# Kernel optimization log

Measured on AMD Instinct MI355X. Metric: run time of the kernel, lower is better.

The kernel has to match this reference:

```python
import jax, jax.numpy as jnp
import numpy as np


def setup_inputs() -> dict:
    key = jax.random.key(0)
    inputs = jax.random.normal(key, (4096, 8192), dtype=jnp.float32)
    return {"inputs": inputs, "k": 512}


def reference(inputs, k):
    # Original: kth_smallest = sort_ascending(inputs)[..., n-1-k]
    # i.e. the (k+1)-th largest value per row. Equivalent via top_k.
    # Keep only elements STRICTLY greater than that threshold.
    thresh = jax.lax.top_k(inputs, k + 1)[0][..., -1]  # [batch]
    mask = (inputs > thresh[:, None]).astype(inputs.dtype)
    return inputs * mask
```

## Files before the change

kernel.cpp:

```cpp
#include <hip/hip_runtime.h>
#include <stdint.h>


constexpr int COLS  = 8192;
constexpr int TPB   = 256;
constexpr int EPT   = COLS / TPB;
constexpr int VPT   = EPT / 4;
constexpr int NBIN0 = 2048;
constexpr int CAP   = 2048;

__device__ __forceinline__ uint32_t map_f32(uint32_t u) {
  return (u & 0x80000000u) ? ~u : (u | 0x80000000u);
}
__device__ __forceinline__ float unmap_f32(uint32_t m) {
  return __uint_as_float((m & 0x80000000u) ? (m ^ 0x80000000u) : ~m);
}
__device__ __forceinline__ uint32_t bin11(uint32_t u) {
  const uint32_t s = u >> 21;
  return (u & 0x80000000u) ? (0x7FFu ^ s) : (s | 0x400u);
}
__device__ __forceinline__ uint32_t hswz(uint32_t w) {
  return w ^ ((w >> 3) & 0x1Cu);
}

__device__ __forceinline__ void bar_lds() {
  asm volatile("s_waitcnt lgkmcnt(0)" ::: "memory");
  __builtin_amdgcn_s_barrier();
  asm volatile("" ::: "memory");
}

template <int RPB>
__global__ __launch_bounds__(TPB, 4)
void ksparse_kernel(const float* __restrict__ in, const int* __restrict__ kptr,
                    float* __restrict__ out) {
  __shared__ __align__(16) uint32_t hist[2 * NBIN0];
  __shared__ uint32_t th[3 * 128];
  __shared__ uint32_t s_packed;
  __shared__ uint32_t s_cnt;
  __shared__ uint32_t s_T;

  const int t    = threadIdx.x;
  const int wave = t >> 6;
  const int lane = t & 63;
  const size_t row0 = (size_t)blockIdx.x * RPB;

  const uint32_t kbase = (uint32_t)(*kptr) + 1u;

  float4 v[2][VPT];

  {
    const float4* inp = (const float4*)(in + row0 * COLS);
#pragma unroll
    for (int i = 0; i < VPT; ++i) v[0][i] = inp[t + i * TPB];
  }

#pragma unroll
  for (int r = 0; r < RPB; ++r) {
    const int cb = r & 1;

    if (r + 1 < RPB) {
      const float4* inp = (const float4*)(in + (row0 + (size_t)(r + 1)) * COLS);
#pragma unroll
      for (int i = 0; i < VPT; ++i) v[cb ^ 1][i] = inp[t + i * TPB];
    }

    uint4* h4 = (uint4*)hist;
#pragma unroll
    for (int i = 0; i < (2 * NBIN0 / 4) / TPB; ++i)
      h4[t + i * TPB] = make_uint4(0u, 0u, 0u, 0u);
    th[t] = 0u;
    if (t < 128) th[256 + t] = 0u;
    if (t == 0) { s_packed = 0u; s_cnt = 0u; }
    bar_lds();

    uint32_t* h = &hist[(wave >> 1) * NBIN0];
#pragma unroll
    for (int i = 0; i < VPT; ++i) {
      atomicAdd(&h[hswz(bin11(__float_as_uint(v[cb][i].x)))], 1u);
      atomicAdd(&h[hswz(bin11(__float_as_uint(v[cb][i].y)))], 1u);
      atomicAdd(&h[hswz(bin11(__float_as_uint(v[cb][i].z)))], 1u);
      atomicAdd(&h[hswz(bin11(__float_as_uint(v[cb][i].w)))], 1u);
    }
    bar_lds();

    if (wave == 0) {
      const uint4* r0 = (const uint4*)&hist[0];
      const uint4* r1 = (const uint4*)&hist[NBIN0];
      uint32_t qs[8];
      uint32_t total = 0;
#pragma unroll
      for (int q = 0; q < 8; ++q) {
        const uint32_t Qs = (uint32_t)(8 * lane + q) ^ (uint32_t)(lane & 7);
        const uint4 a = r0[Qs];
        const uint4 b = r1[Qs];
        qs[q] = (a.x + b.x) + (a.y + b.y) + (a.z + b.z) + (a.w + b.w);
        total += qs[q];
      }
      uint32_t s = total;
#pragma unroll
      for (int off = 1; off < 64; off <<= 1) {
        const uint32_t tmp = __shfl_down(s, off, 64);
        s += (lane + off < 64) ? tmp : 0u;
      }
      const unsigned long long mb = __ballot(s >= kbase);
      const int lstar = 63 - __builtin_clzll(mb);
      if (lane == lstar) {
        uint32_t run = s - total;
        int qq = -1; uint32_t qab = 0;
#pragma unroll
        for (int q = 7; q >= 0; --q) {
          const uint32_t nrun = run + qs[q];
          if (qq < 0 && nrun >= kbase) { qq = q; qab = run; }
          run = nrun;
        }
        const uint32_t Qs = (uint32_t)(8 * lane + qq) ^ (uint32_t)(lane & 7);
        const uint4 a = r0[Qs];
        const uint4 b = r1[Qs];
        const uint32_t c1 = a.y + b.y, c2 = a.z + b.z, c3 = a.w + b.w;
        const uint32_t s3 = qab + c3;
        const uint32_t s2 = s3 + c2, s1 = s2 + c1;
        uint32_t e, above;
        if (s3 >= kbase)      { e = 3u; above = qab; }
        else if (s2 >= kbase) { e = 2u; above = s3; }
        else if (s1 >= kbase) { e = 1u; above = s2; }
        else                  { e = 0u; above = s1; }
        const uint32_t d0 = (uint32_t)(lane * 32 + qq * 4) + e;
        s_packed = (d0 << 14) | above;
      }
    }
    bar_lds();

    const uint32_t pk = s_packed;
    const uint32_t d0 = pk >> 14;

    uint32_t* cand = &hist[NBIN0];
#pragma unroll
    for (int i = 0; i < VPT; ++i) {
      uint32_t u;
      u = __float_as_uint(v[cb][i].x);
      if (bin11(u) == d0) { const uint32_t x = atomicAdd(&s_cnt, 1u); if (x < CAP) cand[x] = map_f32(u) & 0x1FFFFFu; }
      u = __float_as_uint(v[cb][i].y);
      if (bin11(u) == d0) { const uint32_t x = atomicAdd(&s_cnt, 1u); if (x < CAP) cand[x] = map_f32(u) & 0x1FFFFFu; }
      u = __float_as_uint(v[cb][i].z);
      if (bin11(u) == d0) { const uint32_t x = atomicAdd(&s_cnt, 1u); if (x < CAP) cand[x] = map_f32(u) & 0x1FFFFFu; }
      u = __float_as_uint(v[cb][i].w);
      if (bin11(u) == d0) { const uint32_t x = atomicAdd(&s_cnt, 1u); if (x < CAP) cand[x] = map_f32(u) & 0x1FFFFFu; }
    }
    bar_lds();

    if (wave == 0) {
      const uint32_t Cc = (s_cnt < (uint32_t)CAP) ? s_cnt : (uint32_t)CAP;
      uint32_t kk = kbase - (pk & 0x3FFFu);
      uint32_t tpref = 0;
#pragma unroll 1
      for (int j = 0; j < 3; ++j) {
        const int dsh = 14 - 7 * j;
        uint32_t* thj = &th[j * 128];
        for (uint32_t idx = (uint32_t)lane; idx < Cc; idx += 64u) {
          const uint32_t c = cand[idx];
          const bool ok = (j == 0) || ((c >> (dsh + 7)) == tpref);
          if (ok) atomicAdd(&thj[(c >> dsh) & 127u], 1u);
        }
        const uint32_t a = thj[lane], b = thj[64 + lane];
        uint32_t sb = b, sa = a;
#pragma unroll
        for (int off = 1; off < 64; off <<= 1) {
          const uint32_t t1 = __shfl_down(sb, off, 64);
          const uint32_t t2 = __shfl_down(sa, off, 64);
          const bool inr = (lane + off < 64);
          sb += inr ? t1 : 0u;
          sa += inr ? t2 : 0u;
        }
        const uint32_t tb = __shfl(sb, 0, 64);
        sa += tb;
        const unsigned long long mbj = __ballot(sb >= kk);
        uint32_t d, ab;
        if (mbj) {
          const int hb = 63 - __builtin_clzll(mbj);
          const uint32_t nx = __shfl(sb, (hb + 1) & 63, 64);
          d = 64u + (uint32_t)hb;
          ab = (hb == 63) ? 0u : nx;
        } else {
          const unsigned long long ma = __ballot(sa >= kk);
          const int ha = 63 - __builtin_clzll(ma);
          const uint32_t nx = __shfl(sa, (ha + 1) & 63, 64);
          d = (uint32_t)ha;
          ab = (ha == 63) ? tb : nx;
        }
        tpref = (tpref << 7) | d;
        kk -= ab;
      }
      if (lane == 0) s_T = (d0 << 21) | tpref;
    }
    bar_lds();

    const float thr = unmap_f32(s_T);
    float4* op = (float4*)(out + (row0 + (size_t)r) * COLS);
#pragma unroll
    for (int i = 0; i < VPT; ++i) {
      float4 w;
      w.x = (v[cb][i].x > thr) ? v[cb][i].x : 0.0f;
      w.y = (v[cb][i].y > thr) ? v[cb][i].y : 0.0f;
      w.z = (v[cb][i].z > thr) ? v[cb][i].z : 0.0f;
      w.w = (v[cb][i].w > thr) ? v[cb][i].w : 0.0f;
      op[t + i * TPB] = w;
    }
  }
}

extern "C" void kernel_launch(void* const* d_in, const int* in_sizes, int n_in,
                              void* d_out, int out_size, void* d_ws, size_t ws_size,
                              hipStream_t stream) {
  const float* in  = (const float*)d_in[0];
  const int*   k   = (const int*)d_in[1];
  float*       out = (float*)d_out;
  int rows = in_sizes[0] / COLS;
  if (rows < 1) rows = 1;
  if ((rows & 3) == 0) {
    ksparse_kernel<4><<<rows / 4, TPB, 0, stream>>>(in, k, out);
  } else {
    ksparse_kernel<1><<<rows, TPB, 0, stream>>>(in, k, out);
  }
}
```

Measured before the change: 283.0 us.

## Prefetch next row via direct global-to-LDS loads instead of register double buffer

Replaces the register double buffer (two float4[8] arrays per thread) with a 32 KB LDS staging buffer filled by global_load_lds. The next row is issued into LDS once the current row has been read into registers for the histogram, which lowers register pressure. The cost is much more LDS per block, so fewer blocks fit on a CU, and the occupancy hint in launch_bounds is dropped. Correctness now depends on manual vmcnt/lgkmcnt waits, and the vmcnt(8) wait is fragile because it assumes a fixed count of outstanding stores versus loads.

Result: faster. 262.4 us (-7.3%).

```diff
diff --git a/kernel.cpp b/kernel.cpp
--- a/kernel.cpp
+++ b/kernel.cpp
@@ -4,8 +4,7 @@
 
 constexpr int COLS  = 8192;
 constexpr int TPB   = 256;
-constexpr int EPT   = COLS / TPB;
-constexpr int VPT   = EPT / 4;
+constexpr int VPT   = 8;
 constexpr int NBIN0 = 2048;
 constexpr int CAP   = 2048;
 
@@ -29,11 +28,27 @@
   asm volatile("" ::: "memory");
 }
 
+__device__ __forceinline__ void gl2lds16(const float* g, float* l) {
+  __builtin_amdgcn_global_load_lds(
+      (const __attribute__((address_space(1))) void*)g,
+      (__attribute__((address_space(3))) void*)l, 16, 0, 0);
+}
+
+__device__ __forceinline__ void stage_row(const float* __restrict__ rowp,
+                                          float* stage, int wave, int lane) {
+  const float* g = rowp + (wave << 11) + (lane << 2);
+  float* l = stage + (wave << 11);
+#pragma unroll
+  for (int i = 0; i < VPT; ++i)
+    gl2lds16(g + i * 256, l + i * 256);
+}
+
 template <int RPB>
-__global__ __launch_bounds__(TPB, 4)
+__global__ __launch_bounds__(TPB)
 void ksparse_kernel(const float* __restrict__ in, const int* __restrict__ kptr,
                     float* __restrict__ out) {
   __shared__ __align__(16) uint32_t hist[2 * NBIN0];
+  __shared__ __align__(16) float    stage[COLS];
   __shared__ uint32_t th[3 * 128];
   __shared__ uint32_t s_packed;
   __shared__ uint32_t s_cnt;
@@ -46,40 +61,35 @@
 
   const uint32_t kbase = (uint32_t)(*kptr) + 1u;
 
-  float4 v[2][VPT];
-
-  {
-    const float4* inp = (const float4*)(in + row0 * COLS);
-#pragma unroll
-    for (int i = 0; i < VPT; ++i) v[0][i] = inp[t + i * TPB];
-  }
+  stage_row(in + row0 * COLS, stage, wave, lane);
 
 #pragma unroll
   for (int r = 0; r < RPB; ++r) {
-    const int cb = r & 1;
-
-    if (r + 1 < RPB) {
-      const float4* inp = (const float4*)(in + (row0 + (size_t)(r + 1)) * COLS);
-#pragma unroll
-      for (int i = 0; i < VPT; ++i) v[cb ^ 1][i] = inp[t + i * TPB];
-    }
-
     uint4* h4 = (uint4*)hist;
 #pragma unroll
-    for (int i = 0; i < (2 * NBIN0 / 4) / TPB; ++i)
+    for (int i = 0; i < 4; ++i)
       h4[t + i * TPB] = make_uint4(0u, 0u, 0u, 0u);
     th[t] = 0u;
     if (t < 128) th[256 + t] = 0u;
     if (t == 0) { s_packed = 0u; s_cnt = 0u; }
     bar_lds();
 
+    if (r == 0) asm volatile("s_waitcnt vmcnt(0)" ::: "memory");
+
+    float4 v[VPT];
     uint32_t* h = &hist[(wave >> 1) * NBIN0];
+    const float4* sq = (const float4*)stage + (wave << 9) + lane;
 #pragma unroll
     for (int i = 0; i < VPT; ++i) {
-      atomicAdd(&h[hswz(bin11(__float_as_uint(v[cb][i].x)))], 1u);
-      atomicAdd(&h[hswz(bin11(__float_as_uint(v[cb][i].y)))], 1u);
-      atomicAdd(&h[hswz(bin11(__float_as_uint(v[cb][i].z)))], 1u);
-      atomicAdd(&h[hswz(bin11(__float_as_uint(v[cb][i].w)))], 1u);
+      v[i] = sq[i << 6];
+      atomicAdd(&h[hswz(bin11(__float_as_uint(v[i].x)))], 1u);
+      atomicAdd(&h[hswz(bin11(__float_as_uint(v[i].y)))], 1u);
+      atomicAdd(&h[hswz(bin11(__float_as_uint(v[i].z)))], 1u);
+      atomicAdd(&h[hswz(bin11(__float_as_uint(v[i].w)))], 1u);
+    }
+    if (r + 1 < RPB) {
+      asm volatile("s_waitcnt lgkmcnt(0)" ::: "memory");
+      stage_row(in + (row0 + (size_t)(r + 1)) * COLS, stage, wave, lane);
     }
     bar_lds();
 
@@ -137,13 +147,13 @@
 #pragma unroll
     for (int i = 0; i < VPT; ++i) {
       uint32_t u;
-      u = __float_as_uint(v[cb][i].x);
-      if (bin11(u) == d0) { const uint32_t x = atomicAdd(&s_cnt, 1u); if (x < CAP) cand[x] = map_f32(u) & 0x1FFFFFu; }
-      u = __float_as_uint(v[cb][i].y);
-      if (bin11(u) == d0) { const uint32_t x = atomicAdd(&s_cnt, 1u); if (x < CAP) cand[x] = map_f32(u) & 0x1FFFFFu; }
-      u = __float_as_uint(v[cb][i].z);
-      if (bin11(u) == d0) { const uint32_t x = atomicAdd(&s_cnt, 1u); if (x < CAP) cand[x] = map_f32(u) & 0x1FFFFFu; }
-      u = __float_as_uint(v[cb][i].w);
+      u = __float_as_uint(v[i].x);
+      if (bin11(u) == d0) { const uint32_t x = atomicAdd(&s_cnt, 1u); if (x < CAP) cand[x] = map_f32(u) & 0x1FFFFFu; }
+      u = __float_as_uint(v[i].y);
+      if (bin11(u) == d0) { const uint32_t x = atomicAdd(&s_cnt, 1u); if (x < CAP) cand[x] = map_f32(u) & 0x1FFFFFu; }
+      u = __float_as_uint(v[i].z);
+      if (bin11(u) == d0) { const uint32_t x = atomicAdd(&s_cnt, 1u); if (x < CAP) cand[x] = map_f32(u) & 0x1FFFFFu; }
+      u = __float_as_uint(v[i].w);
       if (bin11(u) == d0) { const uint32_t x = atomicAdd(&s_cnt, 1u); if (x < CAP) cand[x] = map_f32(u) & 0x1FFFFFu; }
     }
     bar_lds();
@@ -195,16 +205,17 @@
     bar_lds();
 
     const float thr = unmap_f32(s_T);
-    float4* op = (float4*)(out + (row0 + (size_t)r) * COLS);
+    float4* op = (float4*)(out + (row0 + (size_t)r) * COLS) + (wave << 9) + lane;
 #pragma unroll
     for (int i = 0; i < VPT; ++i) {
       float4 w;
-      w.x = (v[cb][i].x > thr) ? v[cb][i].x : 0.0f;
-      w.y = (v[cb][i].y > thr) ? v[cb][i].y : 0.0f;
-      w.z = (v[cb][i].z > thr) ? v[cb][i].z : 0.0f;
-      w.w = (v[cb][i].w > thr) ? v[cb][i].w : 0.0f;
-      op[t + i * TPB] = w;
-    }
+      w.x = (v[i].x > thr) ? v[i].x : 0.0f;
+      w.y = (v[i].y > thr) ? v[i].y : 0.0f;
+      w.z = (v[i].z > thr) ? v[i].z : 0.0f;
+      w.w = (v[i].w > thr) ? v[i].w : 0.0f;
+      op[i << 6] = w;
+    }
+    asm volatile("s_waitcnt vmcnt(8)" ::: "memory");
   }
 }
 
```
